# Kernel optimization log

Hardware: AMD Instinct MI355X
Metric: run time of the kernel (lower is better)

Reference implementation:

```python
import jax, jax.numpy as jnp
import numpy as np

B, S, D = 2, 2048, 2048
H = 16
KV_RANK, Q_RANK = 512, 1536
NOPE, ROPE_D, VD = 128, 64, 128
QK_D = NOPE + ROPE_D  # 192


def _rope(t, positions):
    # t: (B, H, S, d) with d even; rotate-half RoPE, theta=10000
    d = t.shape[-1]
    inv_freq = 1.0 / (10000.0 ** (jnp.arange(0, d, 2, dtype=jnp.float32) / d))
    ang = positions.astype(jnp.float32)[:, None] * inv_freq  # (S, d//2)
    cos, sin = jnp.cos(ang), jnp.sin(ang)                    # (S, d//2)
    t1, t2 = t[..., : d // 2], t[..., d // 2 :]
    return jnp.concatenate([t1 * cos - t2 * sin, t2 * cos + t1 * sin], axis=-1)


def setup_inputs() -> dict:
    key = jax.random.key(0)
    ks = jax.random.split(key, 10)
    sc = 0.02
    return {
        "x": jax.random.normal(ks[0], (B, S, D), dtype=jnp.float32),
        "positions": jnp.arange(S, dtype=jnp.int32),
        # torch.nn.Linear weights are (out_features, in_features)
        "Wq_down": jax.random.normal(ks[1], (Q_RANK, D), dtype=jnp.float32) * sc,
        "Wq_up": jax.random.normal(ks[2], (H * NOPE, Q_RANK), dtype=jnp.float32) * sc,
        "Wq_rope": jax.random.normal(ks[3], (H * ROPE_D, Q_RANK), dtype=jnp.float32) * sc,
        "Wkv_down": jax.random.normal(ks[4], (KV_RANK, D), dtype=jnp.float32) * sc,
        "Wk_up": jax.random.normal(ks[5], (H * NOPE, KV_RANK), dtype=jnp.float32) * sc,
        "Wv_up": jax.random.normal(ks[6], (H * VD, KV_RANK), dtype=jnp.float32) * sc,
        "Wk_rope": jax.random.normal(ks[7], (ROPE_D, D), dtype=jnp.float32) * sc,
        "Wo": jax.random.normal(ks[8], (D, H * VD), dtype=jnp.float32) * sc,
    }


def reference(x, positions, Wq_down, Wq_up, Wq_rope, Wkv_down, Wk_up, Wv_up, Wk_rope, Wo):
    bsz, seq_len, _ = x.shape

    # Query path: low-rank down, then nope + rope up-projections
    c_q = x @ Wq_down.T                                             # (B, S, Q_RANK)
    q_c = (c_q @ Wq_up.T).reshape(bsz, seq_len, H, NOPE).transpose(0, 2, 1, 3)
    q_r = (c_q @ Wq_rope.T).reshape(bsz, seq_len, H, ROPE_D).transpose(0, 2, 1, 3)
    q_r = _rope(q_r, positions)
    q = jnp.concatenate([q_c, q_r], axis=-1)                        # (B, H, S, QK_D)

    # KV path: shared latent, single rope head broadcast to all heads
    c_kv = x @ Wkv_down.T                                           # (B, S, KV_RANK)
    k_c = (c_kv @ Wk_up.T).reshape(bsz, seq_len, H, NOPE).transpose(0, 2, 1, 3)
    v_c = (c_kv @ Wv_up.T).reshape(bsz, seq_len, H, VD).transpose(0, 2, 1, 3)
    k_r = (x @ Wk_rope.T).reshape(bsz, seq_len, 1, ROPE_D).transpose(0, 2, 1, 3)
    k_r = _rope(k_r, positions)
    k_r = jnp.broadcast_to(k_r, (bsz, H, seq_len, ROPE_D))
    k = jnp.concatenate([k_c, k_r], axis=-1)                        # (B, H, S, QK_D)

    # Causal SDPA, scale = 1/sqrt(total qk head dim)
    scale = 1.0 / math.sqrt(QK_D) if False else QK_D ** -0.5
    scores = jnp.einsum("bhqd,bhkd->bhqk", q, k) * scale
    causal = jnp.tril(jnp.ones((seq_len, seq_len), dtype=bool))
    scores = jnp.where(causal, scores, jnp.finfo(scores.dtype).min)
    attn = jax.nn.softmax(scores, axis=-1)
    out = jnp.einsum("bhqk,bhkd->bhqd", attn, v_c)                  # (B, H, S, VD)

    out = out.transpose(0, 2, 1, 3).reshape(bsz, seq_len, H * VD)
    return out @ Wo.T                                               # (B, S, D)
```

## Files before the change

### kernel.cpp

```cpp
#include <hip/hip_runtime.h>
#include <cmath>

#define SLEN 2048

typedef __bf16 bf16x8 __attribute__((ext_vector_type(8)));
typedef float  f32x4  __attribute__((ext_vector_type(4)));

__device__ inline void gld16(const void* g, void* l) {
    __builtin_amdgcn_global_load_lds(
        (const __attribute__((address_space(1))) void*)(uintptr_t)g,
        (__attribute__((address_space(3))) void*)(unsigned)(uintptr_t)l, 16, 0, 0);
}

struct CvArgs {
    const float* src[9];
    __bf16*      dst[9];
    long         cum[10];
};
__global__ __launch_bounds__(256)
void convert_all(CvArgs a) {
    long i8 = ((long)blockIdx.x * 256 + threadIdx.x) * 8;
    if (i8 >= a.cum[9]) return;
    int s = 0;
#pragma unroll
    for (int k = 1; k < 9; k++) if (i8 >= a.cum[k]) s = k;
    long loc = i8 - a.cum[s];
    const float* sp = a.src[s] + loc;
    float4 u0 = *(const float4*)(sp);
    float4 u1 = *(const float4*)(sp + 4);
    bf16x8 o;
    o[0] = (__bf16)u0.x; o[1] = (__bf16)u0.y; o[2] = (__bf16)u0.z; o[3] = (__bf16)u0.w;
    o[4] = (__bf16)u1.x; o[5] = (__bf16)u1.y; o[6] = (__bf16)u1.z; o[7] = (__bf16)u1.w;
    *(bf16x8*)(a.dst[s] + loc) = o;
}

struct Outs { __bf16* a; __bf16* b; __bf16* c; float* f; };

__global__ __launch_bounds__(256, 3)
void gemm_nt(const __bf16* __restrict__ A, const __bf16* __restrict__ B,
             Outs o, const int* __restrict__ positions,
             int M, int N, int K, int mode, float scale) {
    __shared__ __bf16 As[128 * 64];
    __shared__ __bf16 Bs[128 * 64];
    int tid = threadIdx.x;
    int wave = tid >> 6, lane = tid & 63;
    int lane15 = lane & 15, quad = lane >> 4;
    int ri = lane >> 3, ci = lane & 7;
    int cg = ci ^ ri;
    int m0 = blockIdx.x * 128, n0 = blockIdx.y * 128;
    int wm = (wave & 1) * 64, wn = (wave >> 1) * 64;
    f32x4 acc[4][4] = {};

    for (int k0 = 0; k0 < K; k0 += 64) {
#pragma unroll
        for (int t = 0; t < 4; t++) {
            int rr = wave * 32 + t * 8;
            int r = rr + ri;
            gld16(A + (size_t)(m0 + r) * K + k0 + cg * 8, As + rr * 64);
            int br = n0 + r; if (br > N - 1) br = N - 1;
            gld16(B + (size_t)br * K + k0 + cg * 8, Bs + rr * 64);
        }
        __syncthreads();
#pragma unroll
        for (int kk = 0; kk < 64; kk += 32) {
            int jb = kk >> 3;
            bf16x8 af[4], bfr[4];
#pragma unroll
            for (int mt = 0; mt < 4; mt++) {
                int rA = wm + mt * 16 + lane15;
                af[mt] = *(bf16x8*)(As + rA * 64 + (((jb + quad) ^ (rA & 7)) << 3));
            }
#pragma unroll
            for (int nt = 0; nt < 4; nt++) {
                int rB = wn + nt * 16 + lane15;
                bfr[nt] = *(bf16x8*)(Bs + rB * 64 + (((jb + quad) ^ (rB & 7)) << 3));
            }
#pragma unroll
            for (int mt = 0; mt < 4; mt++)
#pragma unroll
                for (int nt = 0; nt < 4; nt++)
                    acc[mt][nt] = __builtin_amdgcn_mfma_f32_16x16x32_bf16(
                        af[mt], bfr[nt], acc[mt][nt], 0, 0, 0);
        }
        __syncthreads();
    }

    const float KLOG = 13.287712379549449f / 32.0f;

    if (mode == 8 && n0 == 2048) {
        if (wn == 0) {
#pragma unroll
            for (int mt = 0; mt < 4; mt++) {
                int row = m0 + wm + mt * 16 + quad * 4;
#pragma unroll
                for (int nt = 0; nt < 2; nt++) {
                    int i = nt * 16 + lane15;
                    float inv = exp2f(-(float)i * KLOG);
#pragma unroll
                    for (int r = 0; r < 4; r++) {
                        int tok = row + r;
                        float p = (float)positions[tok & (SLEN - 1)];
                        float sn, cs; sincosf(p * inv, &sn, &cs);
                        float t1 = acc[mt][nt][r], t2 = acc[mt][nt + 2][r];
                        float rot1 = t1 * cs - t2 * sn;
                        float rot2 = t2 * cs + t1 * sn;
                        size_t ob = (size_t)tok * 3072 + 128;
#pragma unroll
                        for (int hh = 0; hh < 16; hh++) {
                            o.c[ob + hh * 192 + i]      = (__bf16)rot1;
                            o.c[ob + hh * 192 + 32 + i] = (__bf16)rot2;
                        }
                    }
                }
            }
        }
        return;
    }
    if (mode == 9 && n0 >= 2048) {
        int hh = (n0 + wn - 2048) >> 6;
#pragma unroll
        for (int mt = 0; mt < 4; mt++) {
            int row = m0 + wm + mt * 16 + quad * 4;
#pragma unroll
            for (int nt = 0; nt < 2; nt++) {
                int i = nt * 16 + lane15;
                float inv = exp2f(-(float)i * KLOG);
#pragma unroll
                for (int r = 0; r < 4; r++) {
                    int tok = row + r;
                    float p = (float)positions[tok & (SLEN - 1)];
                    float sn, cs; sincosf(p * inv, &sn, &cs);
                    float t1 = acc[mt][nt][r], t2 = acc[mt][nt + 2][r];
                    size_t ob = (size_t)tok * 3072 + hh * 192 + 128;
                    o.a[ob + i]      = (__bf16)((t1 * cs - t2 * sn) * scale);
                    o.a[ob + 32 + i] = (__bf16)((t2 * cs + t1 * sn) * scale);
                }
            }
        }
        return;
    }

#pragma unroll
    for (int mt = 0; mt < 4; mt++) {
        int row = m0 + wm + mt * 16 + quad * 4;
#pragma unroll
        for (int nt = 0; nt < 4; nt++) {
            int col = n0 + wn + nt * 16 + lane15;
            if (col < N) {
#pragma unroll
                for (int r = 0; r < 4; r++) {
                    float v = acc[mt][nt][r];
                    size_t rw = (size_t)(row + r);
                    if (mode == 2) {
                        o.f[rw * N + col] = v;
                    } else if (mode == 8) {
                        if (col < 1536) o.a[rw * 1536 + col] = (__bf16)v;
                        else            o.b[rw * 512 + col - 1536] = (__bf16)v;
                    } else if (mode == 9) {
                        o.a[rw * 3072 + (col >> 7) * 192 + (col & 127)] =
                            (__bf16)(v * scale);
                    } else {
                        if (col < 2048)
                            o.a[rw * 3072 + (col >> 7) * 192 + (col & 127)] = (__bf16)v;
                        else {
                            int d = col - 2048;
                            o.b[((size_t)d * 2 + (rw >> 11)) * 2048 + (rw & 2047)] = (__bf16)v;
                        }
                    }
                }
            }
        }
    }
}

__global__ __launch_bounds__(256, 2)
void mla_attn(const __bf16* __restrict__ Q, const __bf16* __restrict__ K,
              const __bf16* __restrict__ Vt, __bf16* __restrict__ O) {
    __shared__ __bf16 Ks[64 * 192];
    __shared__ __bf16 Vs[128 * 64];
    __shared__ __bf16 Ps[4][32][72];
    int tid = threadIdx.x, wave = tid >> 6, lane = tid & 63;
    int lane15 = lane & 15, quad = lane >> 4;

    int lin = blockIdx.x + (blockIdx.y << 4) + (blockIdx.z << 8);
    int xcd = lin & 7, slot = lin >> 3;
    int x = slot & 15;
    int g = xcd + ((slot >> 4) << 3);
    int h = g & 15, b = g >> 4;

    int qt0 = (x & 1) ? (x >> 1) : (15 - (x >> 1));
    int qt = b ? (15 - qt0) : qt0;
    int q0 = qt * 128;
    const __bf16* Qb  = Q + (size_t)b * SLEN * 3072 + h * 192;
    const __bf16* Kb  = K + (size_t)b * SLEN * 3072 + h * 192;
    const __bf16* vtb = Vt + ((size_t)(h * 128) * 2 + b) * 2048;

    bf16x8 qf[2][6];
#pragma unroll
    for (int mt = 0; mt < 2; mt++) {
        int qrow = q0 + wave * 32 + mt * 16 + lane15;
#pragma unroll
        for (int kk = 0; kk < 6; kk++)
            qf[mt][kk] = *(const bf16x8*)(Qb + (size_t)qrow * 3072 + kk * 32 + quad * 8);
    }
    bf16x8 ones;
#pragma unroll
    for (int e = 0; e < 8; e++) ones[e] = (__bf16)1.0f;

    f32x4 o_acc[2][8] = {};
    float m_i[2][4], l_i[2][4];
#pragma unroll
    for (int mt = 0; mt < 2; mt++)
#pragma unroll
        for (int r = 0; r < 4; r++) { m_i[mt][r] = -3.0e38f; l_i[mt][r] = 0.0f; }

    for (int j0 = 0; j0 <= q0 + 64; j0 += 64) {
#pragma unroll
        for (int t = 0; t < 6; t++) {
            int sb = (wave * 6 + t) * 64;
            int slot2 = sb + lane;
            int r = slot2 / 24;
            int c = slot2 - r * 24;
            int cgk = (c & ~7) | ((c & 7) ^ (r & 7));
            gld16(Kb + (size_t)(j0 + r) * 3072 + cgk * 8, Ks + sb * 8);
        }
#pragma unroll
        for (int t = 0; t < 4; t++) {
            int sb = (wave * 4 + t) * 64;
            int slot2 = sb + lane;
            int r = slot2 >> 3, c = slot2 & 7;
            gld16(vtb + (size_t)r * 4096 + j0 + (c ^ (r & 7)) * 8, Vs + sb * 8);
        }
        __syncthreads();

        f32x4 acc[2][4] = {};
        __builtin_amdgcn_s_setprio(1);
#pragma unroll
        for (int kk = 0; kk < 6; kk++) {
#pragma unroll
            for (int nt = 0; nt < 4; nt++) {
                int n = nt * 16 + lane15;
                int j = kk * 4 + quad;
                int cl = (j & ~7) | ((j & 7) ^ (n & 7));
                bf16x8 kf = *(bf16x8*)(Ks + n * 192 + cl * 8);
#pragma unroll
                for (int mt = 0; mt < 2; mt++)
                    acc[mt][nt] = __builtin_amdgcn_mfma_f32_16x16x32_bf16(
                        qf[mt][kk], kf, acc[mt][nt], 0, 0, 0);
            }
        }
        __builtin_amdgcn_s_setprio(0);

        if (j0 >= q0) {
#pragma unroll
            for (int mt = 0; mt < 2; mt++) {
                int rowg = q0 + wave * 32 + mt * 16 + quad * 4;
#pragma unroll
                for (int nt = 0; nt < 4; nt++) {
                    int colg = j0 + nt * 16 + lane15;
#pragma unroll
                    for (int r = 0; r < 4; r++)
                        if (colg > rowg + r) acc[mt][nt][r] = -3.0e38f;
                }
            }
        }

        float mx[2][4];
        bool need = false;
#pragma unroll
        for (int mt = 0; mt < 2; mt++)
#pragma unroll
            for (int r = 0; r < 4; r++) {
                float v = fmaxf(fmaxf(acc[mt][0][r], acc[mt][1][r]),
                                fmaxf(acc[mt][2][r], acc[mt][3][r]));
                mx[mt][r] = v;
                need = need || (v > m_i[mt][r] + 24.0f);
            }
        if (__any(need)) {
#pragma unroll
            for (int mt = 0; mt < 2; mt++)
#pragma unroll
                for (int r = 0; r < 4; r++) {
                    float v = mx[mt][r];
#pragma unroll
                    for (int d = 8; d >= 1; d >>= 1) v = fmaxf(v, __shfl_xor(v, d));
                    float mn = fmaxf(m_i[mt][r], v);
                    float alpha = exp2f(m_i[mt][r] - mn);
                    m_i[mt][r] = mn;
                    l_i[mt][r] *= alpha;
#pragma unroll
                    for (int nt = 0; nt < 8; nt++) o_acc[mt][nt][r] *= alpha;
                }
        }

#pragma unroll
        for (int mt = 0; mt < 2; mt++)
#pragma unroll
            for (int r = 0; r < 4; r++)
#pragma unroll
                for (int nt = 0; nt < 4; nt++) {
                    float pp = exp2f(acc[mt][nt][r] - m_i[mt][r]);
                    Ps[wave][mt * 16 + quad * 4 + r][nt * 16 + lane15] = (__bf16)pp;
                }

        f32x4 rs[2] = {};
        __builtin_amdgcn_s_setprio(1);
#pragma unroll
        for (int ks = 0; ks < 2; ks++) {
            bf16x8 pf[2];
#pragma unroll
            for (int mt = 0; mt < 2; mt++)
                pf[mt] = *(bf16x8*)(&Ps[wave][mt * 16 + lane15][ks * 32 + quad * 8]);
#pragma unroll
            for (int nt = 0; nt < 8; nt++) {
                int nn = nt * 16 + lane15;
                int j = ks * 4 + quad;
                bf16x8 vf = *(bf16x8*)(Vs + nn * 64 + (j ^ (nn & 7)) * 8);
#pragma unroll
                for (int mt = 0; mt < 2; mt++)
                    o_acc[mt][nt] = __builtin_amdgcn_mfma_f32_16x16x32_bf16(
                        pf[mt], vf, o_acc[mt][nt], 0, 0, 0);
            }
#pragma unroll
            for (int mt = 0; mt < 2; mt++)
                rs[mt] = __builtin_amdgcn_mfma_f32_16x16x32_bf16(
                    pf[mt], ones, rs[mt], 0, 0, 0);
        }
        __builtin_amdgcn_s_setprio(0);
#pragma unroll
        for (int mt = 0; mt < 2; mt++)
#pragma unroll
            for (int r = 0; r < 4; r++) l_i[mt][r] += rs[mt][r];
        __syncthreads();
    }

    int tokb = b * SLEN + q0 + wave * 32 + quad * 4;
#pragma unroll
    for (int mt = 0; mt < 2; mt++) {
#pragma unroll
        for (int r = 0; r < 4; r++) {
            float inv_l = 1.0f / l_i[mt][r];
            int tok = tokb + mt * 16 + r;
#pragma unroll
            for (int nt = 0; nt < 8; nt++) {
                O[(size_t)tok * 2048 + h * 128 + nt * 16 + lane15] =
                    (__bf16)(o_acc[mt][nt][r] * inv_l);
            }
        }
    }
}

extern "C" void kernel_launch(void* const* d_in, const int* in_sizes, int n_in,
                              void* d_out, int out_size, void* d_ws, size_t ws_size,
                              hipStream_t stream) {
    (void)in_sizes; (void)n_in; (void)out_size; (void)ws_size;
    const int* pos = (const int*)d_in[1];
    float* out = (float*)d_out;

    char* ws = (char*)d_ws;
    size_t off = 0;
    auto alloc = [&](size_t bytes) {
        char* p = ws + off;
        off += (bytes + 255) & ~(size_t)255;
        return p;
    };
    __bf16* x_bf  = (__bf16*)alloc(8388608ull * 2);
    __bf16* Wcat1 = (__bf16*)alloc(4325376ull * 2);
    __bf16* Wcat2 = (__bf16*)alloc(4718592ull * 2);
    __bf16* Wcat3 = (__bf16*)alloc(4194304ull * 2);
    __bf16* Wob   = (__bf16*)alloc(4194304ull * 2);
    __bf16* c_q   = (__bf16*)alloc(4096ull * 1536 * 2);
    __bf16* c_kv  = (__bf16*)alloc(4096ull * 512 * 2);
    __bf16* v_t   = (__bf16*)alloc(4096ull * 2048 * 2);
    __bf16* q_all = (__bf16*)alloc(4096ull * 3072 * 2);
    __bf16* k_all = (__bf16*)alloc(4096ull * 3072 * 2);
    __bf16* attn_o = (__bf16*)c_q;

    const float scale_l2 = 1.4426950408889634f / sqrtf(192.0f);
    dim3 blk(256);

    CvArgs cv;
    cv.src[0] = (const float*)d_in[0]; cv.dst[0] = x_bf;
    cv.src[1] = (const float*)d_in[2]; cv.dst[1] = Wcat1;
    cv.src[2] = (const float*)d_in[5]; cv.dst[2] = Wcat1 + 3145728;
    cv.src[3] = (const float*)d_in[8]; cv.dst[3] = Wcat1 + 4194304;
    cv.src[4] = (const float*)d_in[3]; cv.dst[4] = Wcat2;
    cv.src[5] = (const float*)d_in[4]; cv.dst[5] = Wcat2 + 3145728;
    cv.src[6] = (const float*)d_in[6]; cv.dst[6] = Wcat3;
    cv.src[7] = (const float*)d_in[7]; cv.dst[7] = Wcat3 + 1048576;
    cv.src[8] = (const float*)d_in[9]; cv.dst[8] = Wob;
    long ns[9] = {8388608, 3145728, 1048576, 131072, 3145728, 1572864,
                  1048576, 1048576, 4194304};
    cv.cum[0] = 0;
    for (int i = 0; i < 9; i++) cv.cum[i + 1] = cv.cum[i] + ns[i];
    convert_all<<<dim3((unsigned)(cv.cum[9] / 2048)), blk, 0, stream>>>(cv);

    Outs o1 = { c_q, c_kv, k_all, nullptr };
    gemm_nt<<<dim3(32, 17), blk, 0, stream>>>(x_bf, Wcat1, o1, pos, 4096, 2112, 2048, 8, 1.0f);
    Outs o2 = { q_all, nullptr, nullptr, nullptr };
    gemm_nt<<<dim3(32, 24), blk, 0, stream>>>(c_q, Wcat2, o2, pos, 4096, 3072, 1536, 9, scale_l2);
    Outs o3 = { k_all, v_t, nullptr, nullptr };
    gemm_nt<<<dim3(32, 32), blk, 0, stream>>>(c_kv, Wcat3, o3, pos, 4096, 4096, 512, 10, 1.0f);
    mla_attn<<<dim3(16, 16, 2), blk, 0, stream>>>(q_all, k_all, v_t, attn_o);
    Outs o4 = { nullptr, nullptr, nullptr, out };
    gemm_nt<<<dim3(32, 16), blk, 0, stream>>>(attn_o, Wob, o4, pos, 4096, 2048, 2048, 2, 1.0f);
}
```

Baseline: 417.1 us.

## Halve attention tile sizes to 64-query blocks with 32-key steps for occupancy

Restructures the flash-attention kernel so each block handles 64 query rows (16 per wave) and iterates over 32-key tiles, with V loaded every other step as a 64-column tile. The grid doubles to 1024 blocks and launch bounds request 4 blocks per SM, aiming for more parallelism and better latency hiding via higher occupancy and lower register and LDS use. The cost is less reuse of each K/V tile across queries, twice as many barriers and loop iterations, and more K traffic from global memory.

```diff
diff --git a/kernel.cpp b/kernel.cpp
--- a/kernel.cpp
+++ b/kernel.cpp
@@ -173,179 +173,152 @@
     }
 }
 
-__global__ __launch_bounds__(256, 2)
+__global__ __launch_bounds__(256, 4)
 void mla_attn(const __bf16* __restrict__ Q, const __bf16* __restrict__ K,
               const __bf16* __restrict__ Vt, __bf16* __restrict__ O) {
-    __shared__ __bf16 Ks[64 * 192];
+    __shared__ __bf16 Ks[32 * 192];
     __shared__ __bf16 Vs[128 * 64];
-    __shared__ __bf16 Ps[4][32][72];
+    __shared__ __bf16 Ps[4][16][40];
     int tid = threadIdx.x, wave = tid >> 6, lane = tid & 63;
     int lane15 = lane & 15, quad = lane >> 4;
 
-    int lin = blockIdx.x + (blockIdx.y << 4) + (blockIdx.z << 8);
+    int lin = blockIdx.x + (blockIdx.y << 5) + (blockIdx.z << 9);
     int xcd = lin & 7, slot = lin >> 3;
-    int x = slot & 15;
-    int g = xcd + ((slot >> 4) << 3);
+    int x = slot & 31;
+    int g = xcd + ((slot >> 5) << 3);
     int h = g & 15, b = g >> 4;
 
-    int qt0 = (x & 1) ? (x >> 1) : (15 - (x >> 1));
-    int qt = b ? (15 - qt0) : qt0;
-    int q0 = qt * 128;
+    int qt0 = (x & 1) ? (x >> 1) : (31 - (x >> 1));
+    int qt = b ? (31 - qt0) : qt0;
+    int q0 = qt * 64;
     const __bf16* Qb  = Q + (size_t)b * SLEN * 3072 + h * 192;
     const __bf16* Kb  = K + (size_t)b * SLEN * 3072 + h * 192;
     const __bf16* vtb = Vt + ((size_t)(h * 128) * 2 + b) * 2048;
 
-    bf16x8 qf[2][6];
-#pragma unroll
-    for (int mt = 0; mt < 2; mt++) {
-        int qrow = q0 + wave * 32 + mt * 16 + lane15;
+    bf16x8 qf[6];
+    {
+        int qrow = q0 + wave * 16 + lane15;
 #pragma unroll
         for (int kk = 0; kk < 6; kk++)
-            qf[mt][kk] = *(const bf16x8*)(Qb + (size_t)qrow * 3072 + kk * 32 + quad * 8);
+            qf[kk] = *(const bf16x8*)(Qb + (size_t)qrow * 3072 + kk * 32 + quad * 8);
     }
     bf16x8 ones;
 #pragma unroll
     for (int e = 0; e < 8; e++) ones[e] = (__bf16)1.0f;
 
-    f32x4 o_acc[2][8] = {};
-    float m_i[2][4], l_i[2][4];
-#pragma unroll
-    for (int mt = 0; mt < 2; mt++)
-#pragma unroll
-        for (int r = 0; r < 4; r++) { m_i[mt][r] = -3.0e38f; l_i[mt][r] = 0.0f; }
-
-    for (int j0 = 0; j0 <= q0 + 64; j0 += 64) {
-#pragma unroll
-        for (int t = 0; t < 6; t++) {
-            int sb = (wave * 6 + t) * 64;
-            int slot2 = sb + lane;
-            int r = slot2 / 24;
-            int c = slot2 - r * 24;
+    f32x4 o_acc[8] = {};
+    float m_i[4], l_i[4];
+#pragma unroll
+    for (int r = 0; r < 4; r++) { m_i[r] = -3.0e38f; l_i[r] = 0.0f; }
+
+    int ntiles = 2 * qt + 2;
+    for (int t = 0; t < ntiles; t++) {
+        int j0 = t * 32;
+#pragma unroll
+        for (int tt = 0; tt < 3; tt++) {
+            int sb = (wave * 3 + tt) * 64;
+            int sl = sb + lane;
+            int r = sl / 24;
+            int c = sl - r * 24;
             int cgk = (c & ~7) | ((c & 7) ^ (r & 7));
             gld16(Kb + (size_t)(j0 + r) * 3072 + cgk * 8, Ks + sb * 8);
         }
-#pragma unroll
-        for (int t = 0; t < 4; t++) {
-            int sb = (wave * 4 + t) * 64;
-            int slot2 = sb + lane;
-            int r = slot2 >> 3, c = slot2 & 7;
-            gld16(vtb + (size_t)r * 4096 + j0 + (c ^ (r & 7)) * 8, Vs + sb * 8);
+        if (!(t & 1)) {
+#pragma unroll
+            for (int tt = 0; tt < 4; tt++) {
+                int sb = (wave * 4 + tt) * 64;
+                int sl = sb + lane;
+                int r = sl >> 3, c = sl & 7;
+                gld16(vtb + (size_t)r * 4096 + j0 + (c ^ (r & 7)) * 8, Vs + sb * 8);
+            }
         }
         __syncthreads();
 
-        f32x4 acc[2][4] = {};
+        f32x4 acc[2] = {};
         __builtin_amdgcn_s_setprio(1);
 #pragma unroll
         for (int kk = 0; kk < 6; kk++) {
 #pragma unroll
-            for (int nt = 0; nt < 4; nt++) {
+            for (int nt = 0; nt < 2; nt++) {
                 int n = nt * 16 + lane15;
                 int j = kk * 4 + quad;
                 int cl = (j & ~7) | ((j & 7) ^ (n & 7));
                 bf16x8 kf = *(bf16x8*)(Ks + n * 192 + cl * 8);
-#pragma unroll
-                for (int mt = 0; mt < 2; mt++)
-                    acc[mt][nt] = __builtin_amdgcn_mfma_f32_16x16x32_bf16(
-                        qf[mt][kk], kf, acc[mt][nt], 0, 0, 0);
+                acc[nt] = __builtin_amdgcn_mfma_f32_16x16x32_bf16(
+                    qf[kk], kf, acc[nt], 0, 0, 0);
             }
         }
         __builtin_amdgcn_s_setprio(0);
 
         if (j0 >= q0) {
-#pragma unroll
-            for (int mt = 0; mt < 2; mt++) {
-                int rowg = q0 + wave * 32 + mt * 16 + quad * 4;
-#pragma unroll
-                for (int nt = 0; nt < 4; nt++) {
-                    int colg = j0 + nt * 16 + lane15;
-#pragma unroll
-                    for (int r = 0; r < 4; r++)
-                        if (colg > rowg + r) acc[mt][nt][r] = -3.0e38f;
-                }
-            }
-        }
-
-        float mx[2][4];
+            int rowg = q0 + wave * 16 + quad * 4;
+#pragma unroll
+            for (int nt = 0; nt < 2; nt++) {
+                int colg = j0 + nt * 16 + lane15;
+#pragma unroll
+                for (int r = 0; r < 4; r++)
+                    if (colg > rowg + r) acc[nt][r] = -3.0e38f;
+            }
+        }
+
+        float mx[4];
         bool need = false;
 #pragma unroll
-        for (int mt = 0; mt < 2; mt++)
+        for (int r = 0; r < 4; r++) {
+            float v = fmaxf(acc[0][r], acc[1][r]);
+            mx[r] = v;
+            need = need || (v > m_i[r] + 24.0f);
+        }
+        if (__any(need)) {
 #pragma unroll
             for (int r = 0; r < 4; r++) {
-                float v = fmaxf(fmaxf(acc[mt][0][r], acc[mt][1][r]),
-                                fmaxf(acc[mt][2][r], acc[mt][3][r]));
-                mx[mt][r] = v;
-                need = need || (v > m_i[mt][r] + 24.0f);
-            }
-        if (__any(need)) {
-#pragma unroll
-            for (int mt = 0; mt < 2; mt++)
-#pragma unroll
-                for (int r = 0; r < 4; r++) {
-                    float v = mx[mt][r];
-#pragma unroll
-                    for (int d = 8; d >= 1; d >>= 1) v = fmaxf(v, __shfl_xor(v, d));
-                    float mn = fmaxf(m_i[mt][r], v);
-                    float alpha = exp2f(m_i[mt][r] - mn);
-                    m_i[mt][r] = mn;
-                    l_i[mt][r] *= alpha;
-#pragma unroll
-                    for (int nt = 0; nt < 8; nt++) o_acc[mt][nt][r] *= alpha;
-                }
-        }
-
-#pragma unroll
-        for (int mt = 0; mt < 2; mt++)
-#pragma unroll
-            for (int r = 0; r < 4; r++)
-#pragma unroll
-                for (int nt = 0; nt < 4; nt++) {
-                    float pp = exp2f(acc[mt][nt][r] - m_i[mt][r]);
-                    Ps[wave][mt * 16 + quad * 4 + r][nt * 16 + lane15] = (__bf16)pp;
-                }
-
-        f32x4 rs[2] = {};
+                float v = mx[r];
+#pragma unroll
+                for (int d = 8; d >= 1; d >>= 1) v = fmaxf(v, __shfl_xor(v, d));
+                float mn = fmaxf(m_i[r], v);
+                float alpha = exp2f(m_i[r] - mn);
+                m_i[r] = mn;
+                l_i[r] *= alpha;
+#pragma unroll
+                for (int nt = 0; nt < 8; nt++) o_acc[nt][r] *= alpha;
+            }
+        }
+
+#pragma unroll
+        for (int r = 0; r < 4; r++)
+#pragma unroll
+            for (int nt = 0; nt < 2; nt++) {
+                float pp = exp2f(acc[nt][r] - m_i[r]);
+                Ps[wave][quad * 4 + r][nt * 16 + lane15] = (__bf16)pp;
+            }
+
+        f32x4 rs = {};
         __builtin_amdgcn_s_setprio(1);
-#pragma unroll
-        for (int ks = 0; ks < 2; ks++) {
-            bf16x8 pf[2];
-#pragma unroll
-            for (int mt = 0; mt < 2; mt++)
-                pf[mt] = *(bf16x8*)(&Ps[wave][mt * 16 + lane15][ks * 32 + quad * 8]);
-#pragma unroll
-            for (int nt = 0; nt < 8; nt++) {
-                int nn = nt * 16 + lane15;
-                int j = ks * 4 + quad;
-                bf16x8 vf = *(bf16x8*)(Vs + nn * 64 + (j ^ (nn & 7)) * 8);
-#pragma unroll
-                for (int mt = 0; mt < 2; mt++)
-                    o_acc[mt][nt] = __builtin_amdgcn_mfma_f32_16x16x32_bf16(
-                        pf[mt], vf, o_acc[mt][nt], 0, 0, 0);
-            }
-#pragma unroll
-            for (int mt = 0; mt < 2; mt++)
-                rs[mt] = __builtin_amdgcn_mfma_f32_16x16x32_bf16(
-                    pf[mt], ones, rs[mt], 0, 0, 0);
-        }
+        bf16x8 pf = *(bf16x8*)(&Ps[wave][lane15][quad * 8]);
+        int j = ((t & 1) << 2) + quad;
+#pragma unroll
+        for (int nt = 0; nt < 8; nt++) {
+            int nn = nt * 16 + lane15;
+            bf16x8 vf = *(bf16x8*)(Vs + nn * 64 + ((j ^ (nn & 7)) * 8));
+            o_acc[nt] = __builtin_amdgcn_mfma_f32_16x16x32_bf16(
+                pf, vf, o_acc[nt], 0, 0, 0);
+        }
+        rs = __builtin_amdgcn_mfma_f32_16x16x32_bf16(pf, ones, rs, 0, 0, 0);
         __builtin_amdgcn_s_setprio(0);
 #pragma unroll
-        for (int mt = 0; mt < 2; mt++)
-#pragma unroll
-            for (int r = 0; r < 4; r++) l_i[mt][r] += rs[mt][r];
+        for (int r = 0; r < 4; r++) l_i[r] += rs[r];
         __syncthreads();
     }
 
-    int tokb = b * SLEN + q0 + wave * 32 + quad * 4;
-#pragma unroll
-    for (int mt = 0; mt < 2; mt++) {
-#pragma unroll
-        for (int r = 0; r < 4; r++) {
-            float inv_l = 1.0f / l_i[mt][r];
-            int tok = tokb + mt * 16 + r;
-#pragma unroll
-            for (int nt = 0; nt < 8; nt++) {
-                O[(size_t)tok * 2048 + h * 128 + nt * 16 + lane15] =
-                    (__bf16)(o_acc[mt][nt][r] * inv_l);
-            }
+    int tokb = b * SLEN + q0 + wave * 16 + quad * 4;
+#pragma unroll
+    for (int r = 0; r < 4; r++) {
+        float inv_l = 1.0f / l_i[r];
+        int tok = tokb + r;
+#pragma unroll
+        for (int nt = 0; nt < 8; nt++) {
+            O[(size_t)tok * 2048 + h * 128 + nt * 16 + lane15] =
+                (__bf16)(o_acc[nt][r] * inv_l);
         }
     }
 }
@@ -401,7 +374,7 @@
     gemm_nt<<<dim3(32, 24), blk, 0, stream>>>(c_q, Wcat2, o2, pos, 4096, 3072, 1536, 9, scale_l2);
     Outs o3 = { k_all, v_t, nullptr, nullptr };
     gemm_nt<<<dim3(32, 32), blk, 0, stream>>>(c_kv, Wcat3, o3, pos, 4096, 4096, 512, 10, 1.0f);
-    mla_attn<<<dim3(16, 16, 2), blk, 0, stream>>>(q_all, k_all, v_t, attn_o);
+    mla_attn<<<dim3(32, 16, 2), blk, 0, stream>>>(q_all, k_all, v_t, attn_o);
     Outs o4 = { nullptr, nullptr, nullptr, out };
     gemm_nt<<<dim3(32, 16), blk, 0, stream>>>(attn_o, Wob, o4, pos, 4096, 2048, 2048, 2, 1.0f);
 }
```

Result: no change. 417.9 us (+0.2%).

## Load attention K/V fragments directly from global memory instead of LDS staging

Applied to the files above, without the earlier changes.

The attention kernel drops its shared-memory K and V tiles and the block-wide barriers, and reads the MFMA operand fragments straight from global memory (relying on L1/L2 caching). This removes LDS staging traffic and synchronisation, and the LDS it frees could allow more resident blocks. In exchange, the four waves each issue their own global loads for the same K/V tiles, with strided access patterns that have higher latency. The GEMM is also split into a device body function plus a wrapper, which is only a refactor.

```diff
diff --git a/kernel.cpp b/kernel.cpp
--- a/kernel.cpp
+++ b/kernel.cpp
@@ -36,18 +36,17 @@
 
 struct Outs { __bf16* a; __bf16* b; __bf16* c; float* f; };
 
-__global__ __launch_bounds__(256, 3)
-void gemm_nt(const __bf16* __restrict__ A, const __bf16* __restrict__ B,
-             Outs o, const int* __restrict__ positions,
-             int M, int N, int K, int mode, float scale) {
-    __shared__ __bf16 As[128 * 64];
-    __shared__ __bf16 Bs[128 * 64];
+__device__ __forceinline__ void gemm_body(
+    const __bf16* __restrict__ A, const __bf16* __restrict__ B,
+    Outs o, const int* __restrict__ positions,
+    int N, int K, int mode, float scale, int m0, int n0,
+    __bf16* As, __bf16* Bs)
+{
     int tid = threadIdx.x;
     int wave = tid >> 6, lane = tid & 63;
     int lane15 = lane & 15, quad = lane >> 4;
     int ri = lane >> 3, ci = lane & 7;
     int cg = ci ^ ri;
-    int m0 = blockIdx.x * 128, n0 = blockIdx.y * 128;
     int wm = (wave & 1) * 64, wn = (wave >> 1) * 64;
     f32x4 acc[4][4] = {};
 
@@ -173,11 +172,19 @@
     }
 }
 
+__global__ __launch_bounds__(256, 3)
+void gemm_nt(const __bf16* __restrict__ A, const __bf16* __restrict__ B,
+             Outs o, const int* __restrict__ positions,
+             int N, int K, int mode, float scale) {
+    __shared__ __bf16 As[128 * 64];
+    __shared__ __bf16 Bs[128 * 64];
+    gemm_body(A, B, o, positions, N, K, mode, scale,
+              blockIdx.x * 128, blockIdx.y * 128, As, Bs);
+}
+
 __global__ __launch_bounds__(256, 2)
 void mla_attn(const __bf16* __restrict__ Q, const __bf16* __restrict__ K,
               const __bf16* __restrict__ Vt, __bf16* __restrict__ O) {
-    __shared__ __bf16 Ks[64 * 192];
-    __shared__ __bf16 Vs[128 * 64];
     __shared__ __bf16 Ps[4][32][72];
     int tid = threadIdx.x, wave = tid >> 6, lane = tid & 63;
     int lane15 = lane & 15, quad = lane >> 4;
@@ -215,24 +222,6 @@
         for (int r = 0; r < 4; r++) { m_i[mt][r] = -3.0e38f; l_i[mt][r] = 0.0f; }
 
     for (int j0 = 0; j0 <= q0 + 64; j0 += 64) {
-#pragma unroll
-        for (int t = 0; t < 6; t++) {
-            int sb = (wave * 6 + t) * 64;
-            int slot2 = sb + lane;
-            int r = slot2 / 24;
-            int c = slot2 - r * 24;
-            int cgk = (c & ~7) | ((c & 7) ^ (r & 7));
-            gld16(Kb + (size_t)(j0 + r) * 3072 + cgk * 8, Ks + sb * 8);
-        }
-#pragma unroll
-        for (int t = 0; t < 4; t++) {
-            int sb = (wave * 4 + t) * 64;
-            int slot2 = sb + lane;
-            int r = slot2 >> 3, c = slot2 & 7;
-            gld16(vtb + (size_t)r * 4096 + j0 + (c ^ (r & 7)) * 8, Vs + sb * 8);
-        }
-        __syncthreads();
-
         f32x4 acc[2][4] = {};
         __builtin_amdgcn_s_setprio(1);
 #pragma unroll
@@ -240,9 +229,8 @@
 #pragma unroll
             for (int nt = 0; nt < 4; nt++) {
                 int n = nt * 16 + lane15;
-                int j = kk * 4 + quad;
-                int cl = (j & ~7) | ((j & 7) ^ (n & 7));
-                bf16x8 kf = *(bf16x8*)(Ks + n * 192 + cl * 8);
+                bf16x8 kf = *(const bf16x8*)(Kb + (size_t)(j0 + n) * 3072 +
+                                             kk * 32 + quad * 8);
 #pragma unroll
                 for (int mt = 0; mt < 2; mt++)
                     acc[mt][nt] = __builtin_amdgcn_mfma_f32_16x16x32_bf16(
@@ -314,8 +302,8 @@
 #pragma unroll
             for (int nt = 0; nt < 8; nt++) {
                 int nn = nt * 16 + lane15;
-                int j = ks * 4 + quad;
-                bf16x8 vf = *(bf16x8*)(Vs + nn * 64 + (j ^ (nn & 7)) * 8);
+                bf16x8 vf = *(const bf16x8*)(vtb + (size_t)nn * 4096 + j0 +
+                                             ks * 32 + quad * 8);
 #pragma unroll
                 for (int mt = 0; mt < 2; mt++)
                     o_acc[mt][nt] = __builtin_amdgcn_mfma_f32_16x16x32_bf16(
@@ -331,7 +319,6 @@
         for (int mt = 0; mt < 2; mt++)
 #pragma unroll
             for (int r = 0; r < 4; r++) l_i[mt][r] += rs[mt][r];
-        __syncthreads();
     }
 
     int tokb = b * SLEN + q0 + wave * 32 + quad * 4;
@@ -396,12 +383,12 @@
     convert_all<<<dim3((unsigned)(cv.cum[9] / 2048)), blk, 0, stream>>>(cv);
 
     Outs o1 = { c_q, c_kv, k_all, nullptr };
-    gemm_nt<<<dim3(32, 17), blk, 0, stream>>>(x_bf, Wcat1, o1, pos, 4096, 2112, 2048, 8, 1.0f);
+    gemm_nt<<<dim3(32, 17), blk, 0, stream>>>(x_bf, Wcat1, o1, pos, 2112, 2048, 8, 1.0f);
     Outs o2 = { q_all, nullptr, nullptr, nullptr };
-    gemm_nt<<<dim3(32, 24), blk, 0, stream>>>(c_q, Wcat2, o2, pos, 4096, 3072, 1536, 9, scale_l2);
+    gemm_nt<<<dim3(32, 24), blk, 0, stream>>>(c_q, Wcat2, o2, pos, 3072, 1536, 9, scale_l2);
     Outs o3 = { k_all, v_t, nullptr, nullptr };
-    gemm_nt<<<dim3(32, 32), blk, 0, stream>>>(c_kv, Wcat3, o3, pos, 4096, 4096, 512, 10, 1.0f);
+    gemm_nt<<<dim3(32, 32), blk, 0, stream>>>(c_kv, Wcat3, o3, pos, 4096, 512, 10, 1.0f);
     mla_attn<<<dim3(16, 16, 2), blk, 0, stream>>>(q_all, k_all, v_t, attn_o);
     Outs o4 = { nullptr, nullptr, nullptr, out };
-    gemm_nt<<<dim3(32, 16), blk, 0, stream>>>(attn_o, Wob, o4, pos, 4096, 2048, 2048, 2, 1.0f);
-}
+    gemm_nt<<<dim3(32, 16), blk, 0, stream>>>(attn_o, Wob, o4, pos, 2048, 2048, 2, 1.0f);
+}
```

After: 571.0 us. 1.37x slower.
